# Kernel optimization log

Hardware: AMD Instinct MI355X
Metric: run time of the kernel (lower is better)

## Reference

```python
import jax, jax.numpy as jnp
import numpy as np

EPS = 1e-5

def _ln(x, s, b):
    m = jnp.mean(x, axis=-1, keepdims=True)
    v = jnp.mean((x - m) ** 2, axis=-1, keepdims=True)
    return (x - m) * jax.lax.rsqrt(v + EPS) * s + b

def _lin(x, w, b):
    # torch nn.Linear: y = x @ w.T + b, w shape (out, in)
    return jnp.einsum('...i,oi->...o', x, w) + b

def _gelu(x):
    return jax.nn.gelu(x, approximate=False)  # torch nn.GELU default (erf)

def setup_inputs() -> dict:
    key = jax.random.key(0)
    L, B, N, P, D, F, H = 4, 16, 8, 64, 128, 128, 8
    ks = jax.random.split(key, 16)
    nrm = lambda k, s: jax.random.normal(k, s, jnp.float32) * 0.02
    return {
        'sequence': jax.random.normal(ks[0], (B, N, P, D), jnp.float32),
        'H_pre': jax.random.normal(ks[1], (L, B, N, P, D), jnp.float32),
        'pro1_w': nrm(ks[2], (L, F, D)), 'pro1_b': jnp.zeros((L, F), jnp.float32),
        'pro2_w': nrm(ks[3], (L, F, D)), 'pro2_b': jnp.zeros((L, F), jnp.float32),
        'ln_cur_s': jnp.ones((L, F), jnp.float32), 'ln_cur_b': jnp.zeros((L, F), jnp.float32),
        'ln_pre_s': jnp.ones((L, F), jnp.float32), 'ln_pre_b': jnp.zeros((L, F), jnp.float32),
        'cur_qkv_w': nrm(ks[4], (L, 3 * H * F, F)), 'cur_qkv_b': jnp.zeros((L, 3 * H * F), jnp.float32),
        'pre_qkv_w': nrm(ks[5], (L, 3 * H * F, F)), 'pre_qkv_b': jnp.zeros((L, 3 * H * F), jnp.float32),
        'alpha': jax.random.uniform(ks[6], (L, 3, H * F), jnp.float32),
        'proj_w': nrm(ks[7], (L, F, H * F)), 'proj_b': jnp.zeros((L, F), jnp.float32),
        'bn1_s': jnp.ones((L, F), jnp.float32), 'bn1_b': jnp.zeros((L, F), jnp.float32),
        'bn2_s': jnp.ones((L, F), jnp.float32), 'bn2_b': jnp.zeros((L, F), jnp.float32),
        'ln_o_s': jnp.ones((L, F), jnp.float32), 'ln_o_b': jnp.zeros((L, F), jnp.float32),
        'ffn_w': nrm(ks[8], (L, F, F)), 'ffn_b': jnp.zeros((L, F), jnp.float32),
    }

def reference(sequence, H_pre, pro1_w, pro1_b, pro2_w, pro2_b, ln_cur_s, ln_cur_b,
              ln_pre_s, ln_pre_b, cur_qkv_w, cur_qkv_b, pre_qkv_w, pre_qkv_b, alpha,
              proj_w, proj_b, bn1_s, bn1_b, bn2_s, bn2_b, ln_o_s, ln_o_b, ffn_w, ffn_b):
    L = H_pre.shape[0]
    F = ffn_w.shape[-1]
    H = cur_qkv_w.shape[1] // (3 * F)
    scale = F ** -0.5  # Recur_self_attn: dim ** -0.5 with dim = ffn_dim

    def qkv(x, w, b):
        y = _lin(x, w, b)                      # (B, N, P, 3*H*F)
        Bq, Nq, Pq, _ = y.shape
        y = y.reshape(Bq, Nq, Pq, 3, H, F)     # matches 'b n (qkv h d)' split order
        y = jnp.transpose(y, (3, 0, 1, 4, 2, 5))  # (3, B, N, H, P, F)
        return y[0], y[1], y[2]

    cur = sequence  # (B, N, P, D); timesteps are independent in this module -> batched over N
    for l in range(L):
        if l == 0:  # only first cell sees last-dim == dim and projects cur
            cur = _ln(_lin(cur, pro1_w[l], pro1_b[l]), ln_cur_s[l], ln_cur_b[l])
        pre = _ln(_lin(H_pre[l], pro2_w[l], pro2_b[l]), ln_pre_s[l], ln_pre_b[l])

        Qc, Kc, Vc = qkv(cur, cur_qkv_w[l], cur_qkv_b[l])
        Qp, Kp, Vp = qkv(pre, pre_qkv_w[l], pre_qkv_b[l])
        a = jax.nn.sigmoid(alpha[l]).reshape(3, H, F)[:, None, None, :, None, :]  # (3,1,1,H,1,F)
        Q = a[0] * Qc + (1.0 - a[0]) * Qp
        K = a[1] * Kc + (1.0 - a[1]) * Kp
        V = a[2] * Vc + (1.0 - a[2]) * Vp

        attn = jax.nn.softmax(jnp.einsum('bnhpf,bnhqf->bnhpq', Q, K) * scale, axis=-1)
        A = jnp.einsum('bnhpq,bnhqf->bnhpf', attn, V)
        A = _ln(A, bn1_s[l], bn1_b[l])
        Bx, Nx, Hx, Px, Fx = A.shape
        A = jnp.transpose(A, (0, 1, 3, 2, 4)).reshape(Bx, Nx, Px, Hx * Fx)  # 'b h n d -> b n (h d)'
        A = _ln(_lin(A, proj_w[l], proj_b[l]), bn2_s[l], bn2_b[l])
        A = A + _gelu(cur)

        O_hat = _ln(cur + A, ln_o_s[l], ln_o_b[l])
        cur = _lin(O_hat, ffn_w[l], ffn_b[l]) + _gelu(O_hat)
    return cur
```

## Files before the change

### kernel.cpp

```cpp
#include <hip/hip_runtime.h>
#include <math.h>

#define EPS 1e-5f


typedef __bf16 bf16x8 __attribute__((ext_vector_type(8)));
typedef __bf16 bf16x4 __attribute__((ext_vector_type(4)));
typedef float f32x4 __attribute__((ext_vector_type(4)));

#define MFMA16 __builtin_amdgcn_mfma_f32_16x16x32_bf16

__device__ __forceinline__ float gelu_f(float x) {
    return 0.5f * x * (1.0f + erff(x * 0.7071067811865476f));
}

__device__ __forceinline__ void gll16(const void* g, void* l) {
    __builtin_amdgcn_global_load_lds(
        (const __attribute__((address_space(1))) void*)g,
        (__attribute__((address_space(3))) void*)l, 16, 0, 0);
}

__device__ __forceinline__ void cvt_store8(void* dst, const float* __restrict__ src) {
    float4 a = ((const float4*)src)[0];
    float4 b = ((const float4*)src)[1];
    bf16x8 v;
    v[0] = (__bf16)a.x; v[1] = (__bf16)a.y; v[2] = (__bf16)a.z; v[3] = (__bf16)a.w;
    v[4] = (__bf16)b.x; v[5] = (__bf16)b.y; v[6] = (__bf16)b.z; v[7] = (__bf16)b.w;
    *(bf16x8*)dst = v;
}

__device__ __forceinline__ int swz(int row, int k0)   { return row * 128 + (k0 ^ ((row & 7) << 3)); }
__device__ __forceinline__ int swz64(int row, int k0) { return row * 64  + (k0 ^ ((row & 7) << 3)); }

__global__ __launch_bounds__(256) void prep_all(
    const float* __restrict__ Wc, const float* __restrict__ bc,
    const float* __restrict__ Wpq, const float* __restrict__ bp,
    const float* __restrict__ alpha,
    __bf16* __restrict__ Wq, float* __restrict__ bq,
    const float* __restrict__ s0, __bf16* __restrict__ d0, int n0,
    const float* __restrict__ s1, __bf16* __restrict__ d1, int n1,
    const float* __restrict__ s2, __bf16* __restrict__ d2, int n2,
    const float* __restrict__ s3, __bf16* __restrict__ d3, int n3)
{
    int b = blockIdx.x;
    if (b < 1536) {
        int idx = b * 256 + threadIdx.x;
        int l = idx / 98304, rem = idx - l * 98304;
        int row = rem >> 5, g = rem & 31, k0 = g << 3;
        int type = row >> 10, hf = row & 1023, h = hf >> 7, f = hf & 127;
        int rowp = h * 384 + type * 128 + f;
        float a = 1.0f / (1.0f + expf(-alpha[l * 3072 + row]));
        __bf16* dst = Wq + ((size_t)l * 3072 + rowp) * 256 + k0;
        if (k0 < 128) {
            const float* s = Wc + ((size_t)l * 3072 + row) * 128 + k0;
#pragma unroll
            for (int j = 0; j < 8; ++j) dst[j] = (__bf16)(a * s[j]);
        } else {
            const float* s = Wpq + ((size_t)l * 3072 + row) * 128 + (k0 - 128);
#pragma unroll
            for (int j = 0; j < 8; ++j) dst[j] = (__bf16)((1.0f - a) * s[j]);
        }
        if (g == 0)
            bq[l * 3072 + rowp] = a * bc[l * 3072 + row] + (1.0f - a) * bp[l * 3072 + row];
    } else {
        int off = ((b - 1536) * 256 + threadIdx.x) * 4;
        const float* s; __bf16* d;
        if (off < n0) { s = s0; d = d0; }
        else {
            off -= n0;
            if (off < n1) { s = s1; d = d1; }
            else {
                off -= n1;
                if (off < n2) { s = s2; d = d2; }
                else {
                    off -= n2;
                    if (off >= n3) return;
                    s = s3; d = d3;
                }
            }
        }
        float4 v = *(const float4*)(s + off);
        d[off] = (__bf16)v.x; d[off + 1] = (__bf16)v.y;
        d[off + 2] = (__bf16)v.z; d[off + 3] = (__bf16)v.w;
    }
}

__global__ __launch_bounds__(256) void lin_all(
    const float* __restrict__ Hpre, const __bf16* __restrict__ pro2b,
    const float* __restrict__ pro2bias,
    const float* __restrict__ lnps, const float* __restrict__ lnpb,
    __bf16* __restrict__ preb,
    const float* __restrict__ seq, const __bf16* __restrict__ pro1b,
    const float* __restrict__ pro1bias,
    const float* __restrict__ lncs, const float* __restrict__ lncb,
    float* __restrict__ curf, __bf16* __restrict__ Xcb)
{
    __shared__ __align__(16) char lds[49152];
    unsigned short* xs = (unsigned short*)lds;
    unsigned short* ws = (unsigned short*)(lds + 16384);
    float* outs = (float*)lds;
    int b = blockIdx.x, t = threadIdx.x;
    const float* x; const __bf16* W; const float* bias;
    const float* lns; const float* lnb;
    float* yf = nullptr; __bf16* Xout; int R;
    if (b < 512) {
        int l = b >> 7; R = (b & 127) * 64;
        x = Hpre + (size_t)l * 8192 * 128;
        W = pro2b + (size_t)l * 16384;
        bias = pro2bias + l * 128; lns = lnps + l * 128; lnb = lnpb + l * 128;
        Xout = preb + (size_t)l * 8192 * 128;
    } else {
        R = (b - 512) * 64;
        x = seq; W = pro1b; bias = pro1bias; lns = lncs; lnb = lncb;
        yf = curf; Xout = Xcb;
    }
#pragma unroll
    for (int i = 0; i < 4; ++i) {
        int c = t + i * 256; int row = c >> 4, k0 = (c & 15) << 3;
        cvt_store8(&xs[swz(row, k0)], x + (size_t)(R + row) * 128 + k0);
    }
#pragma unroll
    for (int i = 0; i < 8; ++i) {
        int c = t + i * 256; int row = c >> 4, k0 = (c & 15) << 3;
        gll16(W + (size_t)row * 128 + (k0 ^ ((row & 7) << 3)), &ws[c * 8]);
    }
    __syncthreads();
    int lane = t & 63, w = t >> 6;
    int wr = w * 16;
    int fr = lane & 15, fk = (lane >> 4) << 3;
    f32x4 acc[8] = {};
#pragma unroll
    for (int kk = 0; kk < 4; ++kk) {
        int k0 = kk * 32 + fk;
        bf16x8 a = *(const bf16x8*)&xs[swz(wr + fr, k0)];
#pragma unroll
        for (int n = 0; n < 8; ++n) {
            bf16x8 bb = *(const bf16x8*)&ws[swz(n * 16 + fr, k0)];
            acc[n] = MFMA16(a, bb, acc[n], 0, 0, 0);
        }
    }
    __syncthreads();
#pragma unroll
    for (int n = 0; n < 8; ++n) {
        int col = n * 16 + fr;
        float bv = bias[col];
        int rl = wr + ((lane >> 4) << 2);
#pragma unroll
        for (int r = 0; r < 4; ++r) outs[(rl + r) * 132 + col] = acc[n][r] + bv;
    }
    __syncthreads();
    int row = t >> 2, oc = t & 3;
    float vals[32]; float s = 0.0f;
#pragma unroll
    for (int i = 0; i < 32; ++i) { vals[i] = outs[row * 132 + oc + 4 * i]; s += vals[i]; }
    s += __shfl_xor(s, 1, 4); s += __shfl_xor(s, 2, 4);
    float mean = s * (1.0f / 128.0f);
    float sq = 0.0f;
#pragma unroll
    for (int i = 0; i < 32; ++i) { float d = vals[i] - mean; sq += d * d; }
    sq += __shfl_xor(sq, 1, 4); sq += __shfl_xor(sq, 2, 4);
    float rs = rsqrtf(sq * (1.0f / 128.0f) + EPS);
#pragma unroll
    for (int i = 0; i < 32; ++i) {
        int c = oc + 4 * i;
        float yv = (vals[i] - mean) * rs * lns[c] + lnb[c];
        if (yf) yf[(size_t)(R + row) * 128 + c] = yv;
        Xout[(size_t)(R + row) * 128 + c] = (__bf16)yv;
    }
}

__global__ __launch_bounds__(256, 2) void qkv_attn(
    const __bf16* __restrict__ Xc, const __bf16* __restrict__ Pre,
    const __bf16* __restrict__ Wq, const float* __restrict__ bq,
    const float* __restrict__ bn1s, const float* __restrict__ bn1b,
    __bf16* __restrict__ At)
{
    __shared__ __align__(16) char lds[81920];
    unsigned short* Xs = (unsigned short*)lds;
    __bf16* Qs  = (__bf16*)lds;
    __bf16* Ks  = (__bf16*)(lds + 16384);
    __bf16* Vts = (__bf16*)(lds + 32768);
    __bf16* Ps  = (__bf16*)lds;

    int bn = blockIdx.x >> 3, h = blockIdx.x & 7;
    int t = threadIdx.x, lane = t & 63, w = t >> 6;
    int fr = lane & 15, fk = (lane >> 4) << 3;
    int rr = (lane >> 4) << 2;
    int w16 = w * 16;
    const __bf16* Wqh = Wq + (size_t)h * 384 * 256;
    const float* bqh = bq + h * 384;
    unsigned short* slab = (unsigned short*)(lds + 32768 + w * 12288);

#pragma unroll
    for (int i = 0; i < 8; ++i) {
        int c = t + i * 256;
        int row = c >> 5, k0 = (c & 31) << 3;
        int ks = k0 ^ ((row & 7) << 3);
        const __bf16* src = (ks < 128)
            ? Xc + (size_t)(bn * 64 + row) * 128 + ks
            : Pre + (size_t)(bn * 64 + row) * 128 + (ks - 128);
        gll16(src, &Xs[c * 8]);
    }
#pragma unroll
    for (int i = 0; i < 12; ++i) {
        int c = lane + i * 64;
        int rl = c >> 3, k0 = (c & 7) << 3;
        gll16(Wqh + (size_t)(w * 96 + rl) * 256 + 0 * 64 + (k0 ^ ((rl & 7) << 3)),
              &slab[c * 8]);
    }
    __syncthreads();

    f32x4 acc[4][6] = {};
    for (int kc = 0; kc < 4; ++kc) {
        if (kc) {
            asm volatile("s_waitcnt lgkmcnt(0)" ::: "memory");
#pragma unroll
            for (int i = 0; i < 12; ++i) {
                int c = lane + i * 64;
                int rl = c >> 3, k0 = (c & 7) << 3;
                gll16(Wqh + (size_t)(w * 96 + rl) * 256 + kc * 64 + (k0 ^ ((rl & 7) << 3)),
                      &slab[c * 8]);
            }
        }
        asm volatile("s_waitcnt vmcnt(0)" ::: "memory");
        __builtin_amdgcn_sched_barrier(0);
#pragma unroll
        for (int kk = 0; kk < 2; ++kk) {
            int kl = kk * 32 + fk;
            int kg = kc * 64 + kl;
            bf16x8 a[4], b[6];
#pragma unroll
            for (int m = 0; m < 4; ++m) {
                int row = m * 16 + fr;
                a[m] = *(const bf16x8*)&Xs[row * 256 + (kg ^ ((fr & 7) << 3))];
            }
#pragma unroll
            for (int n = 0; n < 6; ++n) {
                int rl = n * 16 + fr;
                b[n] = *(const bf16x8*)&slab[rl * 64 + (kl ^ ((fr & 7) << 3))];
            }
            __builtin_amdgcn_s_setprio(1);
#pragma unroll
            for (int m = 0; m < 4; ++m)
#pragma unroll
                for (int n = 0; n < 6; ++n)
                    acc[m][n] = MFMA16(a[m], b[n], acc[m][n], 0, 0, 0);
            __builtin_amdgcn_s_setprio(0);
        }
    }
    __syncthreads();

#pragma unroll
    for (int n = 0; n < 6; ++n) {
        int colb = w * 96 + n * 16;
        int type = colb >> 7;
        float bv = bqh[colb + fr];
        int f = (colb & 127) + fr;
#pragma unroll
        for (int m = 0; m < 4; ++m) {
            if (type == 2) {
                int rbase = m * 16 + rr;
                bf16x4 pk;
#pragma unroll
                for (int r = 0; r < 4; ++r) pk[r] = (__bf16)(acc[m][n][r] + bv);
                *(bf16x4*)&Vts[f * 64 + (rbase ^ ((f & 7) << 3))] = pk;
            } else {
#pragma unroll
                for (int r = 0; r < 4; ++r) {
                    int row = m * 16 + rr + r;
                    float val = acc[m][n][r] + bv;
                    if (type == 0)
                        Qs[row * 128 + (f ^ ((row & 7) << 3))] = (__bf16)val;
                    else
                        Ks[row * 128 + (f ^ ((row & 7) << 3))] = (__bf16)val;
                }
            }
        }
    }
    __syncthreads();

    f32x4 sacc[4] = {};
    __builtin_amdgcn_s_setprio(1);
#pragma unroll
    for (int kk = 0; kk < 4; ++kk) {
        int k0 = kk * 32 + fk;
        int arow = w16 + fr;
        bf16x8 aq = *(const bf16x8*)&Qs[arow * 128 + (k0 ^ ((arow & 7) << 3))];
#pragma unroll
        for (int n = 0; n < 4; ++n) {
            bf16x8 bk = *(const bf16x8*)&Ks[swz(n * 16 + fr, k0)];
            sacc[n] = MFMA16(aq, bk, sacc[n], 0, 0, 0);
        }
    }
    __builtin_amdgcn_s_setprio(0);
    __syncthreads();

    const float scale = 0.08838834764831845f;
#pragma unroll
    for (int r = 0; r < 4; ++r) {
        float sv[4];
#pragma unroll
        for (int n = 0; n < 4; ++n) sv[n] = sacc[n][r] * scale;
        float mx = fmaxf(fmaxf(sv[0], sv[1]), fmaxf(sv[2], sv[3]));
        mx = fmaxf(mx, __shfl_xor(mx, 1, 16));
        mx = fmaxf(mx, __shfl_xor(mx, 2, 16));
        mx = fmaxf(mx, __shfl_xor(mx, 4, 16));
        mx = fmaxf(mx, __shfl_xor(mx, 8, 16));
        float sum = 0.0f;
#pragma unroll
        for (int n = 0; n < 4; ++n) { sv[n] = expf(sv[n] - mx); sum += sv[n]; }
        sum += __shfl_xor(sum, 1, 16);
        sum += __shfl_xor(sum, 2, 16);
        sum += __shfl_xor(sum, 4, 16);
        sum += __shfl_xor(sum, 8, 16);
        float inv = 1.0f / sum;
        int p = w16 + rr + r;
#pragma unroll
        for (int n = 0; n < 4; ++n) {
            int q = n * 16 + fr;
            Ps[p * 64 + (q ^ ((p & 7) << 3))] = (__bf16)(sv[n] * inv);
        }
    }

    f32x4 oacc[8] = {};
    __builtin_amdgcn_s_setprio(1);
#pragma unroll
    for (int kk = 0; kk < 2; ++kk) {
        int k0 = kk * 32 + fk;
        int arow = w16 + fr;
        bf16x8 ap = *(const bf16x8*)&Ps[arow * 64 + (k0 ^ ((arow & 7) << 3))];
#pragma unroll
        for (int n = 0; n < 8; ++n) {
            bf16x8 bv = *(const bf16x8*)&Vts[swz64(n * 16 + fr, k0)];
            oacc[n] = MFMA16(ap, bv, oacc[n], 0, 0, 0);
        }
    }
    __builtin_amdgcn_s_setprio(0);

#pragma unroll
    for (int r = 0; r < 4; ++r) {
        int p = w16 + rr + r;
        float s1 = 0.0f;
#pragma unroll
        for (int n = 0; n < 8; ++n) s1 += oacc[n][r];
        s1 += __shfl_xor(s1, 1, 16);
        s1 += __shfl_xor(s1, 2, 16);
        s1 += __shfl_xor(s1, 4, 16);
        s1 += __shfl_xor(s1, 8, 16);
        float mean = s1 * (1.0f / 128.0f);
        float s2 = 0.0f;
#pragma unroll
        for (int n = 0; n < 8; ++n) { float d = oacc[n][r] - mean; s2 += d * d; }
        s2 += __shfl_xor(s2, 1, 16);
        s2 += __shfl_xor(s2, 2, 16);
        s2 += __shfl_xor(s2, 4, 16);
        s2 += __shfl_xor(s2, 8, 16);
        float rs = rsqrtf(s2 * (1.0f / 128.0f) + EPS);
        __bf16* orow = At + (size_t)(bn * 64 + p) * 1024 + h * 128;
#pragma unroll
        for (int n = 0; n < 8; ++n) {
            int f = n * 16 + fr;
            orow[f] = (__bf16)((oacc[n][r] - mean) * rs * bn1s[f] + bn1b[f]);
        }
    }
}

__global__ __launch_bounds__(256) void proj_ffn_mfma(
    const __bf16* __restrict__ At_g, const __bf16* __restrict__ Wp,
    const float* __restrict__ pb,
    const float* __restrict__ bn2s, const float* __restrict__ bn2b,
    const float* __restrict__ lnos, const float* __restrict__ lnob,
    const __bf16* __restrict__ Wf, const float* __restrict__ fb,
    const float* __restrict__ cur, float* __restrict__ out,
    __bf16* __restrict__ Xcur)
{
    __shared__ __align__(16) char lds[36864];
    unsigned short* ats = (unsigned short*)lds;
    unsigned short* wts = (unsigned short*)(lds + 4096);
    float* outs = (float*)lds;
    int t = threadIdx.x;
    int R = blockIdx.x * 16;
    int lane = t & 63, w = t >> 6;
    int wcol = w * 32;
    int fr = lane & 15, fk = (lane >> 4) << 3;
    int rr = (lane >> 4) << 2;

    f32x4 acc[2] = {};
    for (int kc = 0; kc < 8; ++kc) {
        {
            int row = t >> 4, k0 = (t & 15) << 3;
            gll16(At_g + (size_t)(R + row) * 1024 + kc * 128 + (k0 ^ ((row & 7) << 3)),
                  &ats[t * 8]);
        }
#pragma unroll
        for (int i = 0; i < 8; ++i) {
            int c = t + i * 256; int row = c >> 4, k0 = (c & 15) << 3;
            gll16(Wp + (size_t)row * 1024 + kc * 128 + (k0 ^ ((row & 7) << 3)),
                  &wts[c * 8]);
        }
        __syncthreads();
#pragma unroll
        for (int kk = 0; kk < 4; ++kk) {
            int k0 = kk * 32 + fk;
            bf16x8 a = *(const bf16x8*)&ats[swz(fr, k0)];
#pragma unroll
            for (int n = 0; n < 2; ++n) {
                bf16x8 b = *(const bf16x8*)&wts[swz(wcol + n * 16 + fr, k0)];
                acc[n] = MFMA16(a, b, acc[n], 0, 0, 0);
            }
        }
        __syncthreads();
    }

#pragma unroll
    for (int n = 0; n < 2; ++n) {
        int col = wcol + n * 16 + fr;
        float bv = pb[col];
#pragma unroll
        for (int r = 0; r < 4; ++r) outs[(rr + r) * 132 + col] = acc[n][r] + bv;
    }
    __syncthreads();

    int row = t >> 4, oc = t & 15;
    float vals[8]; float s = 0.0f;
#pragma unroll
    for (int i = 0; i < 8; ++i) { vals[i] = outs[row * 132 + oc + 16 * i]; s += vals[i]; }
    s += __shfl_xor(s, 1, 16); s += __shfl_xor(s, 2, 16);
    s += __shfl_xor(s, 4, 16); s += __shfl_xor(s, 8, 16);
    float mean = s * (1.0f / 128.0f);
    float sq = 0.0f;
#pragma unroll
    for (int i = 0; i < 8; ++i) { float d = vals[i] - mean; sq += d * d; }
    sq += __shfl_xor(sq, 1, 16); sq += __shfl_xor(sq, 2, 16);
    sq += __shfl_xor(sq, 4, 16); sq += __shfl_xor(sq, 8, 16);
    float rs = rsqrtf(sq * (1.0f / 128.0f) + EPS);

    float oh[8]; float s2 = 0.0f;
#pragma unroll
    for (int i = 0; i < 8; ++i) {
        int c = oc + 16 * i;
        float ynorm = (vals[i] - mean) * rs * bn2s[c] + bn2b[c];
        float cv = cur[(size_t)(R + row) * 128 + c];
        oh[i] = cv + (ynorm + gelu_f(cv));
        s2 += oh[i];
    }
    s2 += __shfl_xor(s2, 1, 16); s2 += __shfl_xor(s2, 2, 16);
    s2 += __shfl_xor(s2, 4, 16); s2 += __shfl_xor(s2, 8, 16);
    float mean2 = s2 * (1.0f / 128.0f);
    float sq2 = 0.0f;
#pragma unroll
    for (int i = 0; i < 8; ++i) { float d = oh[i] - mean2; sq2 += d * d; }
    sq2 += __shfl_xor(sq2, 1, 16); sq2 += __shfl_xor(sq2, 2, 16);
    sq2 += __shfl_xor(sq2, 4, 16); sq2 += __shfl_xor(sq2, 8, 16);
    float rs2 = rsqrtf(sq2 * (1.0f / 128.0f) + EPS);
#pragma unroll
    for (int i = 0; i < 8; ++i) {
        int c = oc + 16 * i;
        oh[i] = (oh[i] - mean2) * rs2 * lnos[c] + lnob[c];
    }
    __syncthreads();

#pragma unroll
    for (int i = 0; i < 8; ++i) {
        int c = oc + 16 * i;
        ((__bf16*)ats)[row * 128 + (c ^ ((row & 7) << 3))] = (__bf16)oh[i];
    }
#pragma unroll
    for (int i = 0; i < 8; ++i) {
        int c = t + i * 256; int rw = c >> 4, k0 = (c & 15) << 3;
        gll16(Wf + (size_t)rw * 128 + (k0 ^ ((rw & 7) << 3)), &wts[c * 8]);
    }
    __syncthreads();

    f32x4 acc2[2] = {};
#pragma unroll
    for (int kk = 0; kk < 4; ++kk) {
        int k0 = kk * 32 + fk;
        bf16x8 a = *(const bf16x8*)&ats[swz(fr, k0)];
#pragma unroll
        for (int n = 0; n < 2; ++n) {
            bf16x8 b = *(const bf16x8*)&wts[swz(wcol + n * 16 + fr, k0)];
            acc2[n] = MFMA16(a, b, acc2[n], 0, 0, 0);
        }
    }
#pragma unroll
    for (int n = 0; n < 2; ++n) {
        int col = wcol + n * 16 + fr;
        float bv = fb[col];
#pragma unroll
        for (int r = 0; r < 4; ++r) {
            int ro = rr + r;
            float ov = (float)((__bf16*)ats)[ro * 128 + (col ^ ((ro & 7) << 3))];
            float val = acc2[n][r] + bv + gelu_f(ov);
            size_t gidx = (size_t)(R + ro) * 128 + col;
            out[gidx] = val;
            if (Xcur) Xcur[gidx] = (__bf16)val;
        }
    }
}

extern "C" void kernel_launch(void* const* d_in, const int* in_sizes, int n_in,
                              void* d_out, int out_size, void* d_ws, size_t ws_size,
                              hipStream_t stream)
{
    const float* seq       = (const float*)d_in[0];
    const float* Hpre      = (const float*)d_in[1];
    const float* pro1_w    = (const float*)d_in[2];
    const float* pro1_b    = (const float*)d_in[3];
    const float* pro2_w    = (const float*)d_in[4];
    const float* pro2_b    = (const float*)d_in[5];
    const float* ln_cur_s  = (const float*)d_in[6];
    const float* ln_cur_b  = (const float*)d_in[7];
    const float* ln_pre_s  = (const float*)d_in[8];
    const float* ln_pre_b  = (const float*)d_in[9];
    const float* cur_qkv_w = (const float*)d_in[10];
    const float* cur_qkv_b = (const float*)d_in[11];
    const float* pre_qkv_w = (const float*)d_in[12];
    const float* pre_qkv_b = (const float*)d_in[13];
    const float* alpha     = (const float*)d_in[14];
    const float* proj_w    = (const float*)d_in[15];
    const float* proj_b    = (const float*)d_in[16];
    const float* bn1_s     = (const float*)d_in[17];
    const float* bn1_b     = (const float*)d_in[18];
    const float* bn2_s     = (const float*)d_in[19];
    const float* bn2_b     = (const float*)d_in[20];
    const float* ln_o_s    = (const float*)d_in[21];
    const float* ln_o_b    = (const float*)d_in[22];
    const float* ffn_w     = (const float*)d_in[23];
    const float* ffn_b     = (const float*)d_in[24];

    char* ws = (char*)d_ws;
    __bf16* Wq      = (__bf16*)ws;                 ws += (size_t)4 * 3072 * 256 * 2;
    float*  bq      = (float*)ws;                  ws += (size_t)4 * 3072 * 4;
    __bf16* Wp_bf   = (__bf16*)ws;                 ws += (size_t)4 * 128 * 1024 * 2;
    __bf16* Wf_bf   = (__bf16*)ws;                 ws += (size_t)4 * 128 * 128 * 2;
    __bf16* pro1_bf = (__bf16*)ws;                 ws += (size_t)128 * 128 * 2;
    __bf16* pro2_bf = (__bf16*)ws;                 ws += (size_t)4 * 128 * 128 * 2;
    __bf16* Xc   = (__bf16*)ws;                    ws += (size_t)8192 * 128 * 2;
    __bf16* preb = (__bf16*)ws;                    ws += (size_t)4 * 8192 * 128 * 2;
    float*  cur  = (float*)ws;                     ws += (size_t)8192 * 128 * 4;
    __bf16* Atb  = (__bf16*)ws;                    ws += (size_t)8192 * 1024 * 2;

    prep_all<<<2192, 256, 0, stream>>>(
        cur_qkv_w, cur_qkv_b, pre_qkv_w, pre_qkv_b, alpha, Wq, bq,
        proj_w, Wp_bf, 4 * 128 * 1024,
        ffn_w, Wf_bf, 4 * 128 * 128,
        pro1_w, pro1_bf, 128 * 128,
        pro2_w, pro2_bf, 4 * 128 * 128);
    lin_all<<<640, 256, 0, stream>>>(Hpre, pro2_bf, pro2_b, ln_pre_s, ln_pre_b,
                                     preb, seq, pro1_bf, pro1_b,
                                     ln_cur_s, ln_cur_b, cur, Xc);

    for (int l = 0; l < 4; ++l) {
        qkv_attn<<<1024, 256, 0, stream>>>(
            Xc, preb + (size_t)l * 8192 * 128,
            Wq + (size_t)l * 3072 * 256, bq + l * 3072,
            bn1_s + l * 128, bn1_b + l * 128, Atb);
        float* outp = (l == 3) ? (float*)d_out : cur;
        proj_ffn_mfma<<<512, 256, 0, stream>>>(Atb,
                                               Wp_bf + (size_t)l * 128 * 1024,
                                               proj_b + l * 128,
                                               bn2_s + l * 128, bn2_b + l * 128,
                                               ln_o_s + l * 128, ln_o_b + l * 128,
                                               Wf_bf + (size_t)l * 16384,
                                               ffn_b + l * 128,
                                               cur, outp, (l == 3) ? nullptr : Xc);
    }
}
```

Measured before the change: 221.3 us.

## Preload full A tile and give each wave a private weight slab in proj_ffn

The projection GEMM now loads the whole 16x1024 A tile into LDS once. Each wave streams its own 32-row slice of the projection weight into a private LDS slab, so the per-k-chunk block-wide __syncthreads become wave-local waitcnts. The FFN stage gets separate LDS regions for O_hat and its weights, which removes one barrier, and launch bounds request 2 blocks per SM. LDS grows to 64KB per block, which may limit occupancy, and waiting on vmcnt(0) each iteration leaves little overlap between loads and compute.

```diff
diff --git a/kernel.cpp b/kernel.cpp
--- a/kernel.cpp
+++ b/kernel.cpp
@@ -365,7 +365,7 @@
     }
 }
 
-__global__ __launch_bounds__(256) void proj_ffn_mfma(
+__global__ __launch_bounds__(256, 2) void proj_ffn_mfma(
     const __bf16* __restrict__ At_g, const __bf16* __restrict__ Wp,
     const float* __restrict__ pb,
     const float* __restrict__ bn2s, const float* __restrict__ bn2b,
@@ -374,43 +374,62 @@
     const float* __restrict__ cur, float* __restrict__ out,
     __bf16* __restrict__ Xcur)
 {
-    __shared__ __align__(16) char lds[36864];
+    __shared__ __align__(16) char lds[65536];
     unsigned short* ats = (unsigned short*)lds;
-    unsigned short* wts = (unsigned short*)(lds + 4096);
     float* outs = (float*)lds;
+    __bf16* ohs = (__bf16*)(lds + 16384);
+    unsigned short* wfs = (unsigned short*)(lds + 32768);
     int t = threadIdx.x;
     int R = blockIdx.x * 16;
     int lane = t & 63, w = t >> 6;
     int wcol = w * 32;
     int fr = lane & 15, fk = (lane >> 4) << 3;
     int rr = (lane >> 4) << 2;
+    unsigned short* slab = (unsigned short*)(lds + 32768 + w * 8192);
+
+#pragma unroll
+    for (int i = 0; i < 8; ++i) {
+        int c = t + i * 256;
+        int row = c >> 7, k0 = (c & 127) << 3;
+        gll16(At_g + (size_t)(R + row) * 1024 + (k0 ^ ((row & 7) << 3)), &ats[c * 8]);
+    }
+#pragma unroll
+    for (int i = 0; i < 8; ++i) {
+        int c = lane + i * 64;
+        int rl = c >> 4, k0 = (c & 15) << 3;
+        gll16(Wp + (size_t)(wcol + rl) * 1024 + 0 * 128 + (k0 ^ ((rl & 7) << 3)),
+              &slab[c * 8]);
+    }
+    __syncthreads();
 
     f32x4 acc[2] = {};
     for (int kc = 0; kc < 8; ++kc) {
-        {
-            int row = t >> 4, k0 = (t & 15) << 3;
-            gll16(At_g + (size_t)(R + row) * 1024 + kc * 128 + (k0 ^ ((row & 7) << 3)),
-                  &ats[t * 8]);
-        }
-#pragma unroll
-        for (int i = 0; i < 8; ++i) {
-            int c = t + i * 256; int row = c >> 4, k0 = (c & 15) << 3;
-            gll16(Wp + (size_t)row * 1024 + kc * 128 + (k0 ^ ((row & 7) << 3)),
-                  &wts[c * 8]);
-        }
-        __syncthreads();
+        if (kc) {
+            asm volatile("s_waitcnt lgkmcnt(0)" ::: "memory");
+#pragma unroll
+            for (int i = 0; i < 8; ++i) {
+                int c = lane + i * 64;
+                int rl = c >> 4, k0 = (c & 15) << 3;
+                gll16(Wp + (size_t)(wcol + rl) * 1024 + kc * 128 + (k0 ^ ((rl & 7) << 3)),
+                      &slab[c * 8]);
+            }
+        }
+        asm volatile("s_waitcnt vmcnt(0)" ::: "memory");
+        __builtin_amdgcn_sched_barrier(0);
 #pragma unroll
         for (int kk = 0; kk < 4; ++kk) {
-            int k0 = kk * 32 + fk;
-            bf16x8 a = *(const bf16x8*)&ats[swz(fr, k0)];
-#pragma unroll
-            for (int n = 0; n < 2; ++n) {
-                bf16x8 b = *(const bf16x8*)&wts[swz(wcol + n * 16 + fr, k0)];
-                acc[n] = MFMA16(a, b, acc[n], 0, 0, 0);
-            }
-        }
-        __syncthreads();
-    }
+            int kl = kk * 32 + fk;
+            int kg = kc * 128 + kl;
+            bf16x8 a = *(const bf16x8*)&ats[fr * 1024 + (kg ^ ((fr & 7) << 3))];
+            bf16x8 b0 = *(const bf16x8*)&slab[(fr) * 128 + (kl ^ ((fr & 7) << 3))];
+            bf16x8 b1 = *(const bf16x8*)&slab[(16 + fr) * 128 + (kl ^ (((16 + fr) & 7) << 3))];
+            __builtin_amdgcn_s_setprio(1);
+            acc[0] = MFMA16(a, b0, acc[0], 0, 0, 0);
+            acc[1] = MFMA16(a, b1, acc[1], 0, 0, 0);
+            __builtin_amdgcn_s_setprio(0);
+        }
+    }
+    __syncthreads();
 
 #pragma unroll
     for (int n = 0; n < 2; ++n) {
@@ -458,17 +477,16 @@
         int c = oc + 16 * i;
         oh[i] = (oh[i] - mean2) * rs2 * lnos[c] + lnob[c];
     }
-    __syncthreads();
 
 #pragma unroll
     for (int i = 0; i < 8; ++i) {
         int c = oc + 16 * i;
-        ((__bf16*)ats)[row * 128 + (c ^ ((row & 7) << 3))] = (__bf16)oh[i];
+        ohs[row * 128 + (c ^ ((row & 7) << 3))] = (__bf16)oh[i];
     }
 #pragma unroll
     for (int i = 0; i < 8; ++i) {
         int c = t + i * 256; int rw = c >> 4, k0 = (c & 15) << 3;
-        gll16(Wf + (size_t)rw * 128 + (k0 ^ ((rw & 7) << 3)), &wts[c * 8]);
+        gll16(Wf + (size_t)rw * 128 + (k0 ^ ((rw & 7) << 3)), &wfs[c * 8]);
     }
     __syncthreads();
 
@@ -476,10 +494,10 @@
 #pragma unroll
     for (int kk = 0; kk < 4; ++kk) {
         int k0 = kk * 32 + fk;
-        bf16x8 a = *(const bf16x8*)&ats[swz(fr, k0)];
+        bf16x8 a = *(const bf16x8*)&ohs[fr * 128 + (k0 ^ ((fr & 7) << 3))];
 #pragma unroll
         for (int n = 0; n < 2; ++n) {
-            bf16x8 b = *(const bf16x8*)&wts[swz(wcol + n * 16 + fr, k0)];
+            bf16x8 b = *(const bf16x8*)&wfs[swz(wcol + n * 16 + fr, k0)];
             acc2[n] = MFMA16(a, b, acc2[n], 0, 0, 0);
         }
     }
@@ -490,7 +508,7 @@
 #pragma unroll
         for (int r = 0; r < 4; ++r) {
             int ro = rr + r;
-            float ov = (float)((__bf16*)ats)[ro * 128 + (col ^ ((ro & 7) << 3))];
+            float ov = (float)ohs[ro * 128 + (col ^ ((ro & 7) << 3))];
             float val = acc2[n][r] + bv + gelu_f(ov);
             size_t gidx = (size_t)(R + ro) * 128 + col;
             out[gidx] = val;
```

After: 218.2 us. No clear change (-1.4%).
